# Performance work log

Measured on AMD Instinct MI355X. Metric: run time of the kernel, lower is better.

Reference implementation:

```python
import jax, jax.numpy as jnp
import numpy as np

# dims
B, L, D0, P, K = 4, 512, 640, 128, 16
C, H, NL = 32, 4, 3            # hidden channels, heads, layers
DH = C // H
RAD_IN = P + 2                 # pair feat + bppm + distance
HPT = 0.3                      # high_prob_threshold


def _build_edges(bppm, coords):
    """Backbone + kNN + high-prob edges per sample, deduped, flattened over batch."""
    src_all, dst_all = [], []
    for b in range(B):
        s_bb = np.arange(L - 1); d_bb = np.arange(1, L)
        srcs = [s_bb, d_bb]; dsts = [d_bb, s_bb]
        c = coords[b]
        d2 = ((c[:, None, :] - c[None, :, :]) ** 2).sum(-1)
        nn = np.argsort(d2, axis=1)[:, 1:K + 1]            # exclude self
        s_knn = np.repeat(np.arange(L), K); d_knn = nn.reshape(-1)
        srcs += [s_knn, d_knn]; dsts += [d_knn, s_knn]
        iu, ju = np.triu_indices(L, 2)                      # |i-j| > 1
        m = bppm[b][iu, ju] >= HPT
        hs, hd = iu[m], ju[m]
        srcs += [hs, hd]; dsts += [hd, hs]
        e = np.unique(np.stack([np.concatenate(srcs), np.concatenate(dsts)], 1), axis=0)
        src_all.append(e[:, 0] + b * L); dst_all.append(e[:, 1] + b * L)
    return np.concatenate(src_all).astype(np.int32), np.concatenate(dst_all).astype(np.int32)


def setup_inputs() -> dict:
    rng = np.random.default_rng(0)
    sequence_rep = rng.standard_normal((B, L, D0)).astype(np.float32)
    pair_rep = rng.standard_normal((B, L, L, P)).astype(np.float32)
    u = rng.random((B, L, L)).astype(np.float32)
    bppm = (0.5 * (u + u.transpose(0, 2, 1))) ** 8          # sparse-ish symmetric BPPM
    initial_coords = (10.0 * rng.standard_normal((B, L, 3))).astype(np.float32)
    edge_src, edge_dst = _build_edges(bppm, initial_coords)

    def w(*shape):
        fan = shape[-2] if len(shape) >= 2 else shape[-1]
        return (rng.standard_normal(shape) / np.sqrt(fan)).astype(np.float32)

    inp = dict(
        sequence_rep=jnp.asarray(sequence_rep), pair_rep=jnp.asarray(pair_rep),
        bppm=jnp.asarray(bppm.astype(np.float32)), initial_coords=jnp.asarray(initial_coords),
        edge_src=jnp.asarray(edge_src), edge_dst=jnp.asarray(edge_dst),
        Win0=jnp.asarray(w(D0, C)), Win1=jnp.asarray(w(1, C)),
        Wr1=jnp.asarray(w(NL, RAD_IN, 64)), br1=jnp.zeros((NL, 64), jnp.float32),
        Wr2=jnp.asarray(w(NL, 64, 4 * C)), br2=jnp.zeros((NL, 4 * C), jnp.float32),
        Wm00=jnp.asarray(w(NL, C, C)), Wm01=jnp.asarray(w(NL, C, C)),
        Wm10=jnp.asarray(w(NL, C, C)), Wm11=jnp.asarray(w(NL, C, C)),
        Wq=jnp.asarray(w(NL, C, C)), Wself0=jnp.asarray(w(NL, C, C)), Wself1=jnp.asarray(w(NL, C, C)),
        gamma0=jnp.ones((NL, C), jnp.float32), beta0=jnp.zeros((NL, C), jnp.float32),
        gamma1=jnp.ones((NL, C), jnp.float32), Wout=jnp.asarray(w(C, 1)),
    )
    return inp


def _forward(sequence_rep, pair_rep, bppm, initial_coords,
             Win0, Win1, Wr1, br1, Wr2, br2, Wm00, Wm01, Wm10, Wm11,
             Wq, Wself0, Wself1, gamma0, beta0, gamma1, Wout, edge_src, edge_dst):
    N = B * L
    x = initial_coords.reshape(N, 3)
    h0 = sequence_rep.reshape(N, D0) @ Win0                  # [N,C] degree-0
    h1 = x[:, None, :] * Win1[0][None, :, None]              # [N,C,3] degree-1
    src, dst = edge_src, edge_dst
    rel = x[dst] - x[src]
    r = jnp.sqrt(jnp.sum(rel * rel, -1) + 1e-12)             # [E]
    rhat = rel / (r[:, None] + 1e-8)                         # Y1 spherical harmonic dir
    b_idx, si, di = src // L, src % L, dst % L
    ef = jnp.concatenate([pair_rep[b_idx, si, di], bppm[b_idx, si, di][:, None], r[:, None]], -1)

    for l in range(NL):
        rad = jax.nn.relu(ef @ Wr1[l] + br1[l]) @ Wr2[l] + br2[l]   # [E,4C] radial weights
        w00, w01, w10, w11 = jnp.split(rad, 4, axis=-1)
        h0s, h1s = h0[src], h1[src]
        dot1 = jnp.einsum('ecd,ed->ec', h1s, rhat)                  # deg1 -> deg0 path
        m0 = w00 * (h0s @ Wm00[l]) + w01 * (dot1 @ Wm01[l])          # [E,C]
        m1 = (w11[:, :, None] * jnp.einsum('ecd,cf->efd', h1s, Wm11[l])
              + (w10 * (h0s @ Wm10[l]))[:, :, None] * rhat[:, None, :])  # [E,C,3]
        # multi-head attention over incoming edges
        q = (h0 @ Wq[l]).reshape(N, H, DH)
        k = m0.reshape(-1, H, DH)
        logit = jnp.sum(q[dst] * k, -1) / np.sqrt(DH)                # [E,H]
        mx = jax.ops.segment_max(logit, dst, num_segments=N)
        mx = jnp.where(jnp.isfinite(mx), mx, 0.0)
        a = jnp.exp(logit - mx[dst])
        den = jax.ops.segment_sum(a, dst, num_segments=N)
        alpha = a / (den[dst] + 1e-9)                                # [E,H]
        agg0 = jax.ops.segment_sum(alpha[:, :, None] * k, dst, num_segments=N).reshape(N, C)
        agg1 = jax.ops.segment_sum(alpha[:, :, None, None] * m1.reshape(-1, H, DH, 3),
                                   dst, num_segments=N).reshape(N, C, 3)
        h0 = h0 + agg0 @ Wself0[l]
        h1 = h1 + jnp.einsum('ncd,cf->nfd', agg1, Wself1[l])
        # norms: LayerNorm on deg-0, equivariant norm-gating on deg-1
        mu = h0.mean(-1, keepdims=True)
        h0 = (h0 - mu) / jnp.sqrt(h0.var(-1, keepdims=True) + 1e-5) * gamma0[l] + beta0[l]
        nrm = jnp.sqrt(jnp.sum(h1 * h1, -1) + 1e-12)                 # [N,C]
        nln = (nrm - nrm.mean(-1, keepdims=True)) / jnp.sqrt(nrm.var(-1, keepdims=True) + 1e-5) * gamma1[l]
        h1 = h1 * (nln / (nrm + 1e-8))[:, :, None]
    delta = jnp.einsum('ncd,co->nod', h1, Wout)[:, 0, :]             # fiber_out {'1':1}
    return (x + delta).reshape(B, L, 3)


def reference(sequence_rep, pair_rep, bppm, initial_coords, edge_src, edge_dst,
              Win0, Win1, Wr1, br1, Wr2, br2, Wm00, Wm01, Wm10, Wm11,
              Wq, Wself0, Wself1, gamma0, beta0, gamma1, Wout):
    return _forward(sequence_rep, pair_rep, bppm, initial_coords,
                    Win0, Win1, Wr1, br1, Wr2, br2, Wm00, Wm01, Wm10, Wm11,
                    Wq, Wself0, Wself1, gamma0, beta0, gamma1, Wout, edge_src, edge_dst)
```

## Files before the change

kernel.cpp:

```cpp
#include <hip/hip_runtime.h>
#include <hip/hip_bf16.h>
#include <math.h>

#define BB 4
#define LL 512
#define D0 640
#define PP 128
#define CC 32
#define NLAYER 3
#define NN (BB*LL)
#define RADIN 130

typedef __attribute__((ext_vector_type(8))) short bf16x8;
typedef __attribute__((ext_vector_type(4))) float f32x4;

__device__ __forceinline__ short f2b(float v) {
    __hip_bfloat16 h = __float2bfloat16(v);
    short s; __builtin_memcpy(&s, &h, 2); return s;
}


__global__ __launch_bounds__(64) void k_init_h0(const float* __restrict__ seq,
                                                const float* __restrict__ Win0,
                                                float* __restrict__ h0) {
    const int n = blockIdx.x, lane = threadIdx.x;
    const int c = lane & 31, half = lane >> 5;
    const float* s = seq + (size_t)n * D0;
    float acc = 0.f;
    const int i0 = half * (D0 / 2), i1 = i0 + (D0 / 2);
    for (int i = i0; i < i1; ++i) acc = fmaf(s[i], Win0[i * CC + c], acc);
    acc += __shfl_xor(acc, 32);
    if (lane < 32) h0[n * CC + c] = acc;
}

__global__ void k_init_h1(const float* __restrict__ x, const float* __restrict__ Win1,
                          float* __restrict__ h1, int* __restrict__ deg) {
    int idx = blockIdx.x * blockDim.x + threadIdx.x;
    if (idx < NN) deg[idx] = 0;
    if (idx >= NN * CC) return;
    int n = idx >> 5, c = idx & 31;
    float w = Win1[c];
    const float* xp = x + n * 3;
    float* hp = h1 + (size_t)n * 96 + c * 3;
    hp[0] = xp[0] * w; hp[1] = xp[1] * w; hp[2] = xp[2] * w;
}

__global__ __launch_bounds__(256) void k_edge_setup(
    const int* __restrict__ src, const int* __restrict__ dst,
    const float* __restrict__ x,
    const float* __restrict__ pair, const float* __restrict__ bppm,
    float* __restrict__ rhat, int* __restrict__ deg,
    short* __restrict__ efb, int E)
{
    int e = blockIdx.x * 4 + (threadIdx.x >> 6);
    int lane = threadIdx.x & 63;
    if (e >= E) return;
    int s = src[e], d = dst[e];
    float dx = x[d * 3 + 0] - x[s * 3 + 0];
    float dy = x[d * 3 + 1] - x[s * 3 + 1];
    float dz = x[d * 3 + 2] - x[s * 3 + 2];
    float r = sqrtf(dx * dx + dy * dy + dz * dz + 1e-12f);
    float ir = 1.f / (r + 1e-8f);
    int b = s / LL, si = s % LL, di = d % LL;
    size_t prow = ((size_t)b * LL + si) * LL + di;
    const float* pr = pair + prow * PP;
    short* out = efb + (size_t)e * 160;
    out[lane] = f2b(pr[lane]);
    out[64 + lane] = f2b(pr[64 + lane]);
    if (lane < 32) {
        float v = 0.f;
        if (lane == 0) v = bppm[prow];
        else if (lane == 1) v = r;
        out[128 + lane] = f2b(v);
    }
    if (lane < 3) rhat[e * 3 + lane] = (lane == 0 ? dx : lane == 1 ? dy : dz) * ir;
    if (lane == 0) atomicAdd(&deg[d], 1);
}

__global__ __launch_bounds__(64) void k_scan(const int* __restrict__ deg,
                                             int* __restrict__ rowptr,
                                             int* __restrict__ cursor) {
    const int lane = threadIdx.x;
    const int base = lane * 32;
    int loc[32]; int s = 0;
    for (int i = 0; i < 32; ++i) { loc[i] = deg[base + i]; s += loc[i]; }
    int pre = s;
    for (int off = 1; off < 64; off <<= 1) {
        int t = __shfl_up(pre, off);
        if (lane >= off) pre += t;
    }
    pre -= s;
    int run = pre;
    for (int i = 0; i < 32; ++i) { rowptr[base + i] = run; cursor[base + i] = 0; run += loc[i]; }
    if (lane == 63) rowptr[NN] = run;
}

__global__ void k_scatter(const int* __restrict__ dst, const int* __restrict__ rowptr,
                          int* __restrict__ cursor, int* __restrict__ eperm, int E) {
    int e = blockIdx.x * blockDim.x + threadIdx.x;
    if (e >= E) return;
    int d = dst[e];
    int pos = atomicAdd(&cursor[d], 1);
    eperm[e] = rowptr[d] + pos;
}

__global__ void k_pack(const float* __restrict__ Wr1, const float* __restrict__ Wr2,
                       short* __restrict__ W1p, short* __restrict__ W2p) {
    int t = blockIdx.x * blockDim.x + threadIdx.x;
    const int tot1 = NLAYER * 5 * 4 * 64 * 8;
    const int tot2 = NLAYER * 2 * 8 * 64 * 8;
    if (t < tot1) {
        int j = t & 7; int r = t >> 3;
        int ln = r & 63; r >>= 6;
        int cb = r & 3; r >>= 2;
        int kb = r % 5; int l = r / 5;
        int row = kb * 32 + (ln >> 4) * 8 + j;
        int col = cb * 16 + (ln & 15);
        float v = (row < RADIN) ? Wr1[((size_t)l * RADIN + row) * 64 + col] : 0.f;
        W1p[t] = f2b(v);
    } else if (t < tot1 + tot2) {
        int t2 = t - tot1;
        int j = t2 & 7; int r = t2 >> 3;
        int ln = r & 63; r >>= 6;
        int cb = r & 7; r >>= 3;
        int kb = r & 1; int l = r >> 1;
        int row = kb * 32 + (ln >> 4) * 8 + j;
        int col = cb * 16 + (ln & 15);
        W2p[t2] = f2b(Wr2[((size_t)l * 64 + row) * 128 + col]);
    }
}

__global__ __launch_bounds__(256) void k_nodepre(
    int l, const float* __restrict__ h0, const float* __restrict__ h1,
    const float* __restrict__ Wq, const float* __restrict__ Wm00,
    const float* __restrict__ Wm10, const float* __restrict__ Wm11,
    float* __restrict__ qbuf, float* __restrict__ P00,
    float* __restrict__ P10, float* __restrict__ P11)
{
    __shared__ float sh0[8][32], sh1[8][96];
    const int c = threadIdx.x & 31, hw = threadIdx.x >> 5;
    const int n = blockIdx.x * 8 + hw;
    sh0[hw][c] = h0[n * CC + c];
    const float* hp = h1 + (size_t)n * 96 + c * 3;
    sh1[hw][c * 3 + 0] = hp[0]; sh1[hw][c * 3 + 1] = hp[1]; sh1[hw][c * 3 + 2] = hp[2];
    const float* WqL  = Wq   + l * 1024;
    const float* W00L = Wm00 + l * 1024;
    const float* W10L = Wm10 + l * 1024;
    const float* W11L = Wm11 + l * 1024;
    float q = 0.f, p00 = 0.f, p10 = 0.f, px = 0.f, py = 0.f, pz = 0.f;
    for (int i = 0; i < 32; ++i) {
        float a = sh0[hw][i];
        q   = fmaf(a, WqL[i * 32 + c], q);
        p00 = fmaf(a, W00L[i * 32 + c], p00);
        p10 = fmaf(a, W10L[i * 32 + c], p10);
        float w = W11L[i * 32 + c];
        px = fmaf(sh1[hw][i * 3 + 0], w, px);
        py = fmaf(sh1[hw][i * 3 + 1], w, py);
        pz = fmaf(sh1[hw][i * 3 + 2], w, pz);
    }
    qbuf[n * 32 + c] = q; P00[n * 32 + c] = p00; P10[n * 32 + c] = p10;
    float* pp = P11 + (size_t)n * 96 + c * 3;
    pp[0] = px; pp[1] = py; pp[2] = pz;
}

__global__ __launch_bounds__(256) void k_radedge(
    int l, int E,
    const int* __restrict__ src,
    const float* __restrict__ rhat,
    const short* __restrict__ efb,
    const short* __restrict__ W1p,
    const short* __restrict__ W2p,
    const float* __restrict__ br1,
    const float* __restrict__ br2,
    const float* __restrict__ Wm01,
    const float* __restrict__ h1,
    const float* __restrict__ P00,
    const float* __restrict__ P10,
    const float* __restrict__ P11,
    const int* __restrict__ eperm,
    float* __restrict__ mbuf)
{
    __shared__ short s_hid[4][16][72];
    __shared__ float s_rad[64][132];
    __shared__ float sW[1024];
    const int lane = threadIdx.x & 63, wv = threadIdx.x >> 6;
    const int r16 = lane & 15, q4 = lane >> 4;
    const int eb = blockIdx.x * 64;
    const int e0 = eb + wv * 16;

    for (int i = threadIdx.x; i < 1024; i += 256) sW[i] = Wm01[l * 1024 + i];

    f32x4 acc0 = {0.f,0.f,0.f,0.f}, acc1 = {0.f,0.f,0.f,0.f};
    f32x4 acc2 = {0.f,0.f,0.f,0.f}, acc3 = {0.f,0.f,0.f,0.f};
    int row = e0 + r16; if (row >= E) row = E - 1;
    const short* arow = efb + (size_t)row * 160 + q4 * 8;
    const short* b1b = W1p + (size_t)l * (5 * 4 * 64 * 8) + lane * 8;
    for (int kb = 0; kb < 5; ++kb) {
        bf16x8 af = *(const bf16x8*)(arow + kb * 32);
        const short* bp = b1b + kb * (4 * 64 * 8);
        bf16x8 b0 = *(const bf16x8*)(bp);
        bf16x8 b1v = *(const bf16x8*)(bp + 64 * 8);
        bf16x8 b2v = *(const bf16x8*)(bp + 2 * 64 * 8);
        bf16x8 b3v = *(const bf16x8*)(bp + 3 * 64 * 8);
        acc0 = __builtin_amdgcn_mfma_f32_16x16x32_bf16(af, b0,  acc0, 0, 0, 0);
        acc1 = __builtin_amdgcn_mfma_f32_16x16x32_bf16(af, b1v, acc1, 0, 0, 0);
        acc2 = __builtin_amdgcn_mfma_f32_16x16x32_bf16(af, b2v, acc2, 0, 0, 0);
        acc3 = __builtin_amdgcn_mfma_f32_16x16x32_bf16(af, b3v, acc3, 0, 0, 0);
    }
    {
        f32x4 a[4] = {acc0, acc1, acc2, acc3};
        for (int cb = 0; cb < 4; ++cb) {
            int col = cb * 16 + r16;
            float b = br1[l * 64 + col];
            for (int i = 0; i < 4; ++i) {
                float v = fmaxf(a[cb][i] + b, 0.f);
                s_hid[wv][q4 * 4 + i][col] = f2b(v);
            }
        }
    }
    f32x4 o[8];
    for (int cb = 0; cb < 8; ++cb) { o[cb].x=0.f; o[cb].y=0.f; o[cb].z=0.f; o[cb].w=0.f; }
    const short* b2b = W2p + (size_t)l * (2 * 8 * 64 * 8) + lane * 8;
    for (int kb = 0; kb < 2; ++kb) {
        bf16x8 af = *(const bf16x8*)(&s_hid[wv][r16][kb * 32 + q4 * 8]);
        const short* bp = b2b + kb * (8 * 64 * 8);
        for (int cb = 0; cb < 8; ++cb) {
            bf16x8 bf = *(const bf16x8*)(bp + cb * (64 * 8));
            o[cb] = __builtin_amdgcn_mfma_f32_16x16x32_bf16(af, bf, o[cb], 0, 0, 0);
        }
    }
    for (int cb = 0; cb < 8; ++cb) {
        int col = cb * 16 + r16;
        float b = br2[l * 128 + col];
        for (int i = 0; i < 4; ++i) {
            s_rad[wv * 16 + q4 * 4 + i][col] = o[cb][i] + b;
        }
    }
    __syncthreads();

    const int hw = threadIdx.x >> 5;
    const int c = lane & 31;
    const int base = lane & 32;
    for (int it = 0; it < 8; ++it) {
        const int el = hw * 8 + it;
        const int e = eb + el;
        if (e >= E) break;
        const int s = src[e];
        const float r0 = rhat[e * 3 + 0], r1 = rhat[e * 3 + 1], r2 = rhat[e * 3 + 2];
        const float* hp = h1 + (size_t)s * 96 + c * 3;
        const float dot = hp[0] * r0 + hp[1] * r1 + hp[2] * r2;
        float t1 = 0.f;
        for (int i = 0; i < 32; ++i) {
            float di = __shfl(dot, base + i);
            t1 = fmaf(di, sW[i * 32 + c], t1);
        }
        const float w00 = s_rad[el][c],      w01 = s_rad[el][32 + c];
        const float w10 = s_rad[el][64 + c], w11 = s_rad[el][96 + c];
        const float m0 = fmaf(w00, P00[s * 32 + c], w01 * t1);
        const float u10 = w10 * P10[s * 32 + c];
        const float* pp = P11 + (size_t)s * 96 + c * 3;
        float* mp = mbuf + (size_t)eperm[e] * 128;
        mp[c] = m0;
        mp[32 + c * 3 + 0] = fmaf(w11, pp[0], u10 * r0);
        mp[32 + c * 3 + 1] = fmaf(w11, pp[1], u10 * r1);
        mp[32 + c * 3 + 2] = fmaf(w11, pp[2], u10 * r2);
    }
}

__global__ __launch_bounds__(256) void k_node(
    int l, const int* __restrict__ rowptr,
    const float* __restrict__ mbuf,
    const float* __restrict__ qbuf_in,
    float* __restrict__ h0, float* __restrict__ h1,
    const float* __restrict__ Ws0, const float* __restrict__ Ws1,
    const float* __restrict__ gam0, const float* __restrict__ bet0,
    const float* __restrict__ gam1,
    const float* __restrict__ Wq, const float* __restrict__ Wm00,
    const float* __restrict__ Wm10, const float* __restrict__ Wm11,
    float* __restrict__ qout, float* __restrict__ P00,
    float* __restrict__ P10, float* __restrict__ P11,
    const float* __restrict__ x, const float* __restrict__ Wout,
    float* __restrict__ outp)
{
    const int n = blockIdx.x;
    const int tid = threadIdx.x;
    const int hw = tid >> 5;
    const int c = tid & 31;
    __shared__ float s_part[8][32][6];
    __shared__ float s_a0[32], s_a1[96];
    __shared__ float s_hn[128];

    const float qc = qbuf_in[n * 32 + c];
    const int st = rowptr[n], en = rowptr[n + 1];

    float m_run = -INFINITY, l_run = 0.f;
    float a0 = 0.f, a1x = 0.f, a1y = 0.f, a1z = 0.f;
    for (int idx = st + hw; idx < en; idx += 8) {
        const float* row = mbuf + (size_t)idx * 128;
        const float kc = row[c];
        const float mv0 = row[32 + c * 3 + 0];
        const float mv1 = row[32 + c * 3 + 1];
        const float mv2 = row[32 + c * 3 + 2];
        float p = qc * kc;
        p += __shfl_xor(p, 1); p += __shfl_xor(p, 2); p += __shfl_xor(p, 4);
        const float logit = p * 0.35355339059327373f;
        const float mn = fmaxf(m_run, logit);
        const float sc = __expf(m_run - mn);
        const float w  = __expf(logit - mn);
        l_run = fmaf(l_run, sc, w);
        a0  = fmaf(a0,  sc, w * kc);
        a1x = fmaf(a1x, sc, w * mv0);
        a1y = fmaf(a1y, sc, w * mv1);
        a1z = fmaf(a1z, sc, w * mv2);
        m_run = mn;
    }
    s_part[hw][c][0] = m_run; s_part[hw][c][1] = l_run;
    s_part[hw][c][2] = a0;
    s_part[hw][c][3] = a1x; s_part[hw][c][4] = a1y; s_part[hw][c][5] = a1z;
    __syncthreads();

    if (tid < 32) {
        float M = s_part[0][c][0], L = s_part[0][c][1], A0 = s_part[0][c][2];
        float Ax = s_part[0][c][3], Ay = s_part[0][c][4], Az = s_part[0][c][5];
        for (int k = 1; k < 8; ++k) {
            const float m2 = s_part[k][c][0];
            if (m2 == -INFINITY) continue;
            const float mn = fmaxf(M, m2);
            const float sa = (M == -INFINITY) ? 0.f : __expf(M - mn);
            const float sb = __expf(m2 - mn);
            L  = L  * sa + s_part[k][c][1] * sb;
            A0 = A0 * sa + s_part[k][c][2] * sb;
            Ax = Ax * sa + s_part[k][c][3] * sb;
            Ay = Ay * sa + s_part[k][c][4] * sb;
            Az = Az * sa + s_part[k][c][5] * sb;
            M = mn;
        }
        const float inv = 1.0f / (L + 1e-9f);
        s_a0[c] = A0 * inv;
        s_a1[c * 3 + 0] = Ax * inv;
        s_a1[c * 3 + 1] = Ay * inv;
        s_a1[c * 3 + 2] = Az * inv;
    }
    __syncthreads();

    if (tid < 32) {
        float x0 = h0[n * CC + c];
        {
            const float* W = Ws0 + l * 1024;
            for (int i = 0; i < 32; ++i) x0 = fmaf(s_a0[i], W[i * 32 + c], x0);
        }
        float mu = x0;
        mu += __shfl_xor(mu, 1); mu += __shfl_xor(mu, 2); mu += __shfl_xor(mu, 4);
        mu += __shfl_xor(mu, 8); mu += __shfl_xor(mu, 16);
        mu *= (1.f / 32.f);
        float sq = x0 * x0;
        sq += __shfl_xor(sq, 1); sq += __shfl_xor(sq, 2); sq += __shfl_xor(sq, 4);
        sq += __shfl_xor(sq, 8); sq += __shfl_xor(sq, 16);
        float var = sq * (1.f / 32.f) - mu * mu;
        float h0n = (x0 - mu) * rsqrtf(var + 1e-5f) * gam0[l * 32 + c] + bet0[l * 32 + c];
        s_hn[c] = h0n;
        if (l + 1 < NLAYER) h0[n * CC + c] = h0n;

        const float* hp = h1 + (size_t)n * 96 + c * 3;
        float v0 = hp[0], v1 = hp[1], v2 = hp[2];
        {
            const float* W = Ws1 + l * 1024;
            for (int i = 0; i < 32; ++i) {
                float w = W[i * 32 + c];
                v0 = fmaf(s_a1[i * 3 + 0], w, v0);
                v1 = fmaf(s_a1[i * 3 + 1], w, v1);
                v2 = fmaf(s_a1[i * 3 + 2], w, v2);
            }
        }
        float nrm = sqrtf(v0 * v0 + v1 * v1 + v2 * v2 + 1e-12f);
        float mu2 = nrm;
        mu2 += __shfl_xor(mu2, 1); mu2 += __shfl_xor(mu2, 2); mu2 += __shfl_xor(mu2, 4);
        mu2 += __shfl_xor(mu2, 8); mu2 += __shfl_xor(mu2, 16);
        mu2 *= (1.f / 32.f);
        float sq2 = nrm * nrm;
        sq2 += __shfl_xor(sq2, 1); sq2 += __shfl_xor(sq2, 2); sq2 += __shfl_xor(sq2, 4);
        sq2 += __shfl_xor(sq2, 8); sq2 += __shfl_xor(sq2, 16);
        float var2 = sq2 * (1.f / 32.f) - mu2 * mu2;
        float nln = (nrm - mu2) * rsqrtf(var2 + 1e-5f) * gam1[l * 32 + c];
        float scl = nln / (nrm + 1e-8f);
        float w0 = v0 * scl, w1 = v1 * scl, w2 = v2 * scl;
        s_hn[32 + c * 3 + 0] = w0;
        s_hn[32 + c * 3 + 1] = w1;
        s_hn[32 + c * 3 + 2] = w2;
        if (l + 1 < NLAYER) {
            float* hq = h1 + (size_t)n * 96 + c * 3;
            hq[0] = w0; hq[1] = w1; hq[2] = w2;
        } else {
            const float wo = Wout[c];
            float d0 = w0 * wo, d1 = w1 * wo, d2 = w2 * wo;
            d0 += __shfl_xor(d0, 1); d1 += __shfl_xor(d1, 1); d2 += __shfl_xor(d2, 1);
            d0 += __shfl_xor(d0, 2); d1 += __shfl_xor(d1, 2); d2 += __shfl_xor(d2, 2);
            d0 += __shfl_xor(d0, 4); d1 += __shfl_xor(d1, 4); d2 += __shfl_xor(d2, 4);
            d0 += __shfl_xor(d0, 8); d1 += __shfl_xor(d1, 8); d2 += __shfl_xor(d2, 8);
            d0 += __shfl_xor(d0, 16); d1 += __shfl_xor(d1, 16); d2 += __shfl_xor(d2, 16);
            if (c == 0) {
                outp[n * 3 + 0] = x[n * 3 + 0] + d0;
                outp[n * 3 + 1] = x[n * 3 + 1] + d1;
                outp[n * 3 + 2] = x[n * 3 + 2] + d2;
            }
        }
    }

    if (l + 1 < NLAYER) {
        __syncthreads();
        const int grp = tid >> 5;
        if (grp < 4) {
            const int lp = l + 1;
            if (grp == 0) {
                const float* W = Wq + lp * 1024;
                float acc = 0.f;
                for (int i = 0; i < 32; ++i) acc = fmaf(s_hn[i], W[i * 32 + c], acc);
                qout[n * 32 + c] = acc;
            } else if (grp == 1) {
                const float* W = Wm00 + lp * 1024;
                float acc = 0.f;
                for (int i = 0; i < 32; ++i) acc = fmaf(s_hn[i], W[i * 32 + c], acc);
                P00[n * 32 + c] = acc;
            } else if (grp == 2) {
                const float* W = Wm10 + lp * 1024;
                float acc = 0.f;
                for (int i = 0; i < 32; ++i) acc = fmaf(s_hn[i], W[i * 32 + c], acc);
                P10[n * 32 + c] = acc;
            } else {
                const float* W = Wm11 + lp * 1024;
                float px = 0.f, py = 0.f, pz = 0.f;
                for (int i = 0; i < 32; ++i) {
                    float w = W[i * 32 + c];
                    px = fmaf(s_hn[32 + i * 3 + 0], w, px);
                    py = fmaf(s_hn[32 + i * 3 + 1], w, py);
                    pz = fmaf(s_hn[32 + i * 3 + 2], w, pz);
                }
                float* pp = P11 + (size_t)n * 96 + c * 3;
                pp[0] = px; pp[1] = py; pp[2] = pz;
            }
        }
    }
}

extern "C" void kernel_launch(void* const* d_in, const int* in_sizes, int n_in,
                              void* d_out, int out_size, void* d_ws, size_t ws_size,
                              hipStream_t stream) {
    const float* seq  = (const float*)d_in[0];
    const float* pair = (const float*)d_in[1];
    const float* bppm = (const float*)d_in[2];
    const float* x    = (const float*)d_in[3];
    const int*   src  = (const int*)d_in[4];
    const int*   dst  = (const int*)d_in[5];
    const float* Win0 = (const float*)d_in[6];
    const float* Win1 = (const float*)d_in[7];
    const float* Wr1  = (const float*)d_in[8];
    const float* br1  = (const float*)d_in[9];
    const float* Wr2  = (const float*)d_in[10];
    const float* br2  = (const float*)d_in[11];
    const float* Wm00 = (const float*)d_in[12];
    const float* Wm01 = (const float*)d_in[13];
    const float* Wm10 = (const float*)d_in[14];
    const float* Wm11 = (const float*)d_in[15];
    const float* Wq   = (const float*)d_in[16];
    const float* Ws0  = (const float*)d_in[17];
    const float* Ws1  = (const float*)d_in[18];
    const float* gam0 = (const float*)d_in[19];
    const float* bet0 = (const float*)d_in[20];
    const float* gam1 = (const float*)d_in[21];
    const float* Wout = (const float*)d_in[22];
    const int E = in_sizes[4];

    char* w = (char*)d_ws;
    auto alloc = [&](size_t nbytes) {
        void* p = (void*)w;
        w += (nbytes + 255) & ~(size_t)255;
        return p;
    };
    float* h0    = (float*)alloc((size_t)NN * CC * 4);
    float* h1    = (float*)alloc((size_t)NN * CC * 3 * 4);
    float* rhat  = (float*)alloc((size_t)E * 3 * 4);
    float* mbuf  = (float*)alloc((size_t)E * 128 * 4);
    int* deg     = (int*)alloc((size_t)NN * 4);
    int* rowptr  = (int*)alloc((size_t)(NN + 1) * 4);
    int* cursor  = (int*)alloc((size_t)NN * 4);
    int* eperm   = (int*)alloc((size_t)E * 4);
    short* efb   = (short*)alloc((size_t)E * 160 * 2);
    short* W1p   = (short*)alloc((size_t)NLAYER * 5 * 4 * 64 * 8 * 2);
    short* W2p   = (short*)alloc((size_t)NLAYER * 2 * 8 * 64 * 8 * 2);
    float* qbuf  = (float*)alloc((size_t)NN * 32 * 4);
    float* P00   = (float*)alloc((size_t)NN * 32 * 4);
    float* P10   = (float*)alloc((size_t)NN * 32 * 4);
    float* P11   = (float*)alloc((size_t)NN * 96 * 4);

    const int TB = 256;
    k_init_h0<<<NN, 64, 0, stream>>>(seq, Win0, h0);
    k_init_h1<<<(NN * CC + TB - 1) / TB, TB, 0, stream>>>(x, Win1, h1, deg);
    k_edge_setup<<<(E + 3) / 4, 256, 0, stream>>>(src, dst, x, pair, bppm,
                                                  rhat, deg, efb, E);
    k_scan<<<1, 64, 0, stream>>>(deg, rowptr, cursor);
    k_scatter<<<(E + TB - 1) / TB, TB, 0, stream>>>(dst, rowptr, cursor, eperm, E);
    {
        int tot = NLAYER * 5 * 4 * 64 * 8 + NLAYER * 2 * 8 * 64 * 8;
        k_pack<<<(tot + TB - 1) / TB, TB, 0, stream>>>(Wr1, Wr2, W1p, W2p);
    }
    k_nodepre<<<NN / 8, 256, 0, stream>>>(0, h0, h1, Wq, Wm00, Wm10, Wm11,
                                          qbuf, P00, P10, P11);

    for (int l = 0; l < NLAYER; ++l) {
        k_radedge<<<(E + 63) / 64, 256, 0, stream>>>(l, E, src, rhat, efb, W1p, W2p,
                                                     br1, br2, Wm01, h1,
                                                     P00, P10, P11, eperm, mbuf);
        k_node<<<NN, 256, 0, stream>>>(l, rowptr, mbuf, qbuf, h0, h1,
                                       Ws0, Ws1, gam0, bet0, gam1,
                                       Wq, Wm00, Wm10, Wm11,
                                       qbuf, P00, P10, P11,
                                       x, Wout, (float*)d_out);
    }
}
```

Baseline: 837.1 us.

## Fuse per-edge radial MLP and messages into per-node attention kernel

Merges the per-edge radial-MLP and message kernel into the per-node attention and update kernel. Each node block now gathers its incoming edges through a dst-sorted edge order, computes their radial weights and messages on the fly, and folds them into the online softmax. This drops the E×128 float message buffer and its global write and read traffic, and saves one launch per layer. Node state is double-buffered because other blocks read neighbours' h1 and projections while the node is updated. The trade-off is that MFMA tiles are underfilled for nodes with fewer than 64 edges and work is unbalanced across node blocks.

```diff
diff --git a/kernel.cpp b/kernel.cpp
--- a/kernel.cpp
+++ b/kernel.cpp
@@ -96,12 +96,12 @@
 }
 
 __global__ void k_scatter(const int* __restrict__ dst, const int* __restrict__ rowptr,
-                          int* __restrict__ cursor, int* __restrict__ eperm, int E) {
+                          int* __restrict__ cursor, int* __restrict__ eorder, int E) {
     int e = blockIdx.x * blockDim.x + threadIdx.x;
     if (e >= E) return;
     int d = dst[e];
     int pos = atomicAdd(&cursor[d], 1);
-    eperm[e] = rowptr[d] + pos;
+    eorder[rowptr[d] + pos] = e;
 }
 
 __global__ void k_pack(const float* __restrict__ Wr1, const float* __restrict__ Wr2,
@@ -163,176 +163,168 @@
     pp[0] = px; pp[1] = py; pp[2] = pz;
 }
 
-__global__ __launch_bounds__(256) void k_radedge(
+__global__ __launch_bounds__(256) void k_layer(
     int l, int E,
-    const int* __restrict__ src,
-    const float* __restrict__ rhat,
+    const int* __restrict__ rowptr, const int* __restrict__ eorder,
+    const int* __restrict__ src, const float* __restrict__ rhat,
     const short* __restrict__ efb,
-    const short* __restrict__ W1p,
-    const short* __restrict__ W2p,
-    const float* __restrict__ br1,
-    const float* __restrict__ br2,
+    const short* __restrict__ W1p, const short* __restrict__ W2p,
+    const float* __restrict__ br1, const float* __restrict__ br2,
     const float* __restrict__ Wm01,
-    const float* __restrict__ h1,
-    const float* __restrict__ P00,
-    const float* __restrict__ P10,
-    const float* __restrict__ P11,
-    const int* __restrict__ eperm,
-    float* __restrict__ mbuf)
-{
-    __shared__ short s_hid[4][16][72];
-    __shared__ float s_rad[64][132];
-    __shared__ float sW[1024];
-    const int lane = threadIdx.x & 63, wv = threadIdx.x >> 6;
-    const int r16 = lane & 15, q4 = lane >> 4;
-    const int eb = blockIdx.x * 64;
-    const int e0 = eb + wv * 16;
-
-    for (int i = threadIdx.x; i < 1024; i += 256) sW[i] = Wm01[l * 1024 + i];
-
-    f32x4 acc0 = {0.f,0.f,0.f,0.f}, acc1 = {0.f,0.f,0.f,0.f};
-    f32x4 acc2 = {0.f,0.f,0.f,0.f}, acc3 = {0.f,0.f,0.f,0.f};
-    int row = e0 + r16; if (row >= E) row = E - 1;
-    const short* arow = efb + (size_t)row * 160 + q4 * 8;
-    const short* b1b = W1p + (size_t)l * (5 * 4 * 64 * 8) + lane * 8;
-    for (int kb = 0; kb < 5; ++kb) {
-        bf16x8 af = *(const bf16x8*)(arow + kb * 32);
-        const short* bp = b1b + kb * (4 * 64 * 8);
-        bf16x8 b0 = *(const bf16x8*)(bp);
-        bf16x8 b1v = *(const bf16x8*)(bp + 64 * 8);
-        bf16x8 b2v = *(const bf16x8*)(bp + 2 * 64 * 8);
-        bf16x8 b3v = *(const bf16x8*)(bp + 3 * 64 * 8);
-        acc0 = __builtin_amdgcn_mfma_f32_16x16x32_bf16(af, b0,  acc0, 0, 0, 0);
-        acc1 = __builtin_amdgcn_mfma_f32_16x16x32_bf16(af, b1v, acc1, 0, 0, 0);
-        acc2 = __builtin_amdgcn_mfma_f32_16x16x32_bf16(af, b2v, acc2, 0, 0, 0);
-        acc3 = __builtin_amdgcn_mfma_f32_16x16x32_bf16(af, b3v, acc3, 0, 0, 0);
-    }
-    {
-        f32x4 a[4] = {acc0, acc1, acc2, acc3};
-        for (int cb = 0; cb < 4; ++cb) {
-            int col = cb * 16 + r16;
-            float b = br1[l * 64 + col];
-            for (int i = 0; i < 4; ++i) {
-                float v = fmaxf(a[cb][i] + b, 0.f);
-                s_hid[wv][q4 * 4 + i][col] = f2b(v);
-            }
-        }
-    }
-    f32x4 o[8];
-    for (int cb = 0; cb < 8; ++cb) { o[cb].x=0.f; o[cb].y=0.f; o[cb].z=0.f; o[cb].w=0.f; }
-    const short* b2b = W2p + (size_t)l * (2 * 8 * 64 * 8) + lane * 8;
-    for (int kb = 0; kb < 2; ++kb) {
-        bf16x8 af = *(const bf16x8*)(&s_hid[wv][r16][kb * 32 + q4 * 8]);
-        const short* bp = b2b + kb * (8 * 64 * 8);
-        for (int cb = 0; cb < 8; ++cb) {
-            bf16x8 bf = *(const bf16x8*)(bp + cb * (64 * 8));
-            o[cb] = __builtin_amdgcn_mfma_f32_16x16x32_bf16(af, bf, o[cb], 0, 0, 0);
-        }
-    }
-    for (int cb = 0; cb < 8; ++cb) {
-        int col = cb * 16 + r16;
-        float b = br2[l * 128 + col];
-        for (int i = 0; i < 4; ++i) {
-            s_rad[wv * 16 + q4 * 4 + i][col] = o[cb][i] + b;
-        }
-    }
-    __syncthreads();
-
-    const int hw = threadIdx.x >> 5;
-    const int c = lane & 31;
-    const int base = lane & 32;
-    for (int it = 0; it < 8; ++it) {
-        const int el = hw * 8 + it;
-        const int e = eb + el;
-        if (e >= E) break;
-        const int s = src[e];
-        const float r0 = rhat[e * 3 + 0], r1 = rhat[e * 3 + 1], r2 = rhat[e * 3 + 2];
-        const float* hp = h1 + (size_t)s * 96 + c * 3;
-        const float dot = hp[0] * r0 + hp[1] * r1 + hp[2] * r2;
-        float t1 = 0.f;
-        for (int i = 0; i < 32; ++i) {
-            float di = __shfl(dot, base + i);
-            t1 = fmaf(di, sW[i * 32 + c], t1);
-        }
-        const float w00 = s_rad[el][c],      w01 = s_rad[el][32 + c];
-        const float w10 = s_rad[el][64 + c], w11 = s_rad[el][96 + c];
-        const float m0 = fmaf(w00, P00[s * 32 + c], w01 * t1);
-        const float u10 = w10 * P10[s * 32 + c];
-        const float* pp = P11 + (size_t)s * 96 + c * 3;
-        float* mp = mbuf + (size_t)eperm[e] * 128;
-        mp[c] = m0;
-        mp[32 + c * 3 + 0] = fmaf(w11, pp[0], u10 * r0);
-        mp[32 + c * 3 + 1] = fmaf(w11, pp[1], u10 * r1);
-        mp[32 + c * 3 + 2] = fmaf(w11, pp[2], u10 * r2);
-    }
-}
-
-__global__ __launch_bounds__(256) void k_node(
-    int l, const int* __restrict__ rowptr,
-    const float* __restrict__ mbuf,
-    const float* __restrict__ qbuf_in,
-    float* __restrict__ h0, float* __restrict__ h1,
+    const float* __restrict__ h1_in,
+    const float* __restrict__ P00, const float* __restrict__ P10,
+    const float* __restrict__ P11, const float* __restrict__ qbuf_in,
+    float* __restrict__ h0,
+    float* __restrict__ h1_out,
     const float* __restrict__ Ws0, const float* __restrict__ Ws1,
     const float* __restrict__ gam0, const float* __restrict__ bet0,
     const float* __restrict__ gam1,
     const float* __restrict__ Wq, const float* __restrict__ Wm00,
     const float* __restrict__ Wm10, const float* __restrict__ Wm11,
-    float* __restrict__ qout, float* __restrict__ P00,
-    float* __restrict__ P10, float* __restrict__ P11,
+    float* __restrict__ qout, float* __restrict__ P00o,
+    float* __restrict__ P10o, float* __restrict__ P11o,
     const float* __restrict__ x, const float* __restrict__ Wout,
     float* __restrict__ outp)
 {
     const int n = blockIdx.x;
     const int tid = threadIdx.x;
-    const int hw = tid >> 5;
-    const int c = tid & 31;
-    __shared__ float s_part[8][32][6];
+    const int lane = tid & 63, wv = tid >> 6;
+    const int r16 = lane & 15, q4 = lane >> 4;
+    const int hw = tid >> 5, c = tid & 31;
+
+    __shared__ short s_hid[4][16][72];
+    __shared__ float s_rad[64][132];
+    __shared__ float sW[1024];
+    __shared__ int   s_eid[64];
     __shared__ float s_a0[32], s_a1[96];
     __shared__ float s_hn[128];
-
+#define S_PART(k, cc, j) (((float*)s_rad)[(((k) * 32 + (cc)) * 6) + (j)])
+
+    for (int i = tid; i < 1024; i += 256) sW[i] = Wm01[l * 1024 + i];
+
+    const int st = rowptr[n], en = rowptr[n + 1];
     const float qc = qbuf_in[n * 32 + c];
-    const int st = rowptr[n], en = rowptr[n + 1];
+
+    const short* b1b = W1p + (size_t)l * (5 * 4 * 64 * 8) + lane * 8;
+    const short* b2b = W2p + (size_t)l * (2 * 8 * 64 * 8) + lane * 8;
 
     float m_run = -INFINITY, l_run = 0.f;
     float a0 = 0.f, a1x = 0.f, a1y = 0.f, a1z = 0.f;
-    for (int idx = st + hw; idx < en; idx += 8) {
-        const float* row = mbuf + (size_t)idx * 128;
-        const float kc = row[c];
-        const float mv0 = row[32 + c * 3 + 0];
-        const float mv1 = row[32 + c * 3 + 1];
-        const float mv2 = row[32 + c * 3 + 2];
-        float p = qc * kc;
-        p += __shfl_xor(p, 1); p += __shfl_xor(p, 2); p += __shfl_xor(p, 4);
-        const float logit = p * 0.35355339059327373f;
-        const float mn = fmaxf(m_run, logit);
-        const float sc = __expf(m_run - mn);
-        const float w  = __expf(logit - mn);
-        l_run = fmaf(l_run, sc, w);
-        a0  = fmaf(a0,  sc, w * kc);
-        a1x = fmaf(a1x, sc, w * mv0);
-        a1y = fmaf(a1y, sc, w * mv1);
-        a1z = fmaf(a1z, sc, w * mv2);
-        m_run = mn;
-    }
-    s_part[hw][c][0] = m_run; s_part[hw][c][1] = l_run;
-    s_part[hw][c][2] = a0;
-    s_part[hw][c][3] = a1x; s_part[hw][c][4] = a1y; s_part[hw][c][5] = a1z;
+
+    for (int t0 = st; t0 < en; t0 += 64) {
+        __syncthreads();
+        if (tid < 64) {
+            int slot = t0 + tid;
+            s_eid[tid] = eorder[slot < en ? slot : en - 1];
+        }
+        __syncthreads();
+
+        f32x4 acc0 = {0.f,0.f,0.f,0.f}, acc1 = {0.f,0.f,0.f,0.f};
+        f32x4 acc2 = {0.f,0.f,0.f,0.f}, acc3 = {0.f,0.f,0.f,0.f};
+        {
+            const int eid = s_eid[wv * 16 + r16];
+            const short* arow = efb + (size_t)eid * 160 + q4 * 8;
+            for (int kb = 0; kb < 5; ++kb) {
+                bf16x8 af = *(const bf16x8*)(arow + kb * 32);
+                const short* bp = b1b + kb * (4 * 64 * 8);
+                bf16x8 b0 = *(const bf16x8*)(bp);
+                bf16x8 b1v = *(const bf16x8*)(bp + 64 * 8);
+                bf16x8 b2v = *(const bf16x8*)(bp + 2 * 64 * 8);
+                bf16x8 b3v = *(const bf16x8*)(bp + 3 * 64 * 8);
+                acc0 = __builtin_amdgcn_mfma_f32_16x16x32_bf16(af, b0,  acc0, 0, 0, 0);
+                acc1 = __builtin_amdgcn_mfma_f32_16x16x32_bf16(af, b1v, acc1, 0, 0, 0);
+                acc2 = __builtin_amdgcn_mfma_f32_16x16x32_bf16(af, b2v, acc2, 0, 0, 0);
+                acc3 = __builtin_amdgcn_mfma_f32_16x16x32_bf16(af, b3v, acc3, 0, 0, 0);
+            }
+        }
+        {
+            f32x4 a[4] = {acc0, acc1, acc2, acc3};
+            for (int cb = 0; cb < 4; ++cb) {
+                int col = cb * 16 + r16;
+                float b = br1[l * 64 + col];
+                for (int i = 0; i < 4; ++i) {
+                    float v = fmaxf(a[cb][i] + b, 0.f);
+                    s_hid[wv][q4 * 4 + i][col] = f2b(v);
+                }
+            }
+        }
+        f32x4 o[8];
+        for (int cb = 0; cb < 8; ++cb) { o[cb].x=0.f; o[cb].y=0.f; o[cb].z=0.f; o[cb].w=0.f; }
+        for (int kb = 0; kb < 2; ++kb) {
+            bf16x8 af = *(const bf16x8*)(&s_hid[wv][r16][kb * 32 + q4 * 8]);
+            const short* bp = b2b + kb * (8 * 64 * 8);
+            for (int cb = 0; cb < 8; ++cb) {
+                bf16x8 bf = *(const bf16x8*)(bp + cb * (64 * 8));
+                o[cb] = __builtin_amdgcn_mfma_f32_16x16x32_bf16(af, bf, o[cb], 0, 0, 0);
+            }
+        }
+        for (int cb = 0; cb < 8; ++cb) {
+            int col = cb * 16 + r16;
+            float b = br2[l * 128 + col];
+            for (int i = 0; i < 4; ++i) {
+                s_rad[wv * 16 + q4 * 4 + i][col] = o[cb][i] + b;
+            }
+        }
+        __syncthreads();
+
+        const int base = lane & 32;
+        for (int it = 0; it < 8; ++it) {
+            const int el = hw * 8 + it;
+            const int slot = t0 + el;
+            if (slot >= en) break;
+            const int e = s_eid[el];
+            const int s = src[e];
+            const float r0 = rhat[e * 3 + 0], r1 = rhat[e * 3 + 1], r2 = rhat[e * 3 + 2];
+            const float* hp = h1_in + (size_t)s * 96 + c * 3;
+            const float dot = hp[0] * r0 + hp[1] * r1 + hp[2] * r2;
+            float t1 = 0.f;
+            for (int i = 0; i < 32; ++i) {
+                float di = __shfl(dot, base + i);
+                t1 = fmaf(di, sW[i * 32 + c], t1);
+            }
+            const float w00 = s_rad[el][c],      w01 = s_rad[el][32 + c];
+            const float w10 = s_rad[el][64 + c], w11 = s_rad[el][96 + c];
+            const float kc = fmaf(w00, P00[s * 32 + c], w01 * t1);
+            const float u10 = w10 * P10[s * 32 + c];
+            const float* pp = P11 + (size_t)s * 96 + c * 3;
+            const float mv0 = fmaf(w11, pp[0], u10 * r0);
+            const float mv1 = fmaf(w11, pp[1], u10 * r1);
+            const float mv2 = fmaf(w11, pp[2], u10 * r2);
+            float p = qc * kc;
+            p += __shfl_xor(p, 1); p += __shfl_xor(p, 2); p += __shfl_xor(p, 4);
+            const float logit = p * 0.35355339059327373f;
+            const float mn = fmaxf(m_run, logit);
+            const float sc = __expf(m_run - mn);
+            const float w  = __expf(logit - mn);
+            l_run = fmaf(l_run, sc, w);
+            a0  = fmaf(a0,  sc, w * kc);
+            a1x = fmaf(a1x, sc, w * mv0);
+            a1y = fmaf(a1y, sc, w * mv1);
+            a1z = fmaf(a1z, sc, w * mv2);
+            m_run = mn;
+        }
+    }
+
     __syncthreads();
+    S_PART(hw, c, 0) = m_run; S_PART(hw, c, 1) = l_run;
+    S_PART(hw, c, 2) = a0;
+    S_PART(hw, c, 3) = a1x; S_PART(hw, c, 4) = a1y; S_PART(hw, c, 5) = a1z;
+    __syncthreads();
 
     if (tid < 32) {
-        float M = s_part[0][c][0], L = s_part[0][c][1], A0 = s_part[0][c][2];
-        float Ax = s_part[0][c][3], Ay = s_part[0][c][4], Az = s_part[0][c][5];
+        float M = S_PART(0, c, 0), L = S_PART(0, c, 1), A0 = S_PART(0, c, 2);
+        float Ax = S_PART(0, c, 3), Ay = S_PART(0, c, 4), Az = S_PART(0, c, 5);
         for (int k = 1; k < 8; ++k) {
-            const float m2 = s_part[k][c][0];
+            const float m2 = S_PART(k, c, 0);
             if (m2 == -INFINITY) continue;
             const float mn = fmaxf(M, m2);
             const float sa = (M == -INFINITY) ? 0.f : __expf(M - mn);
             const float sb = __expf(m2 - mn);
-            L  = L  * sa + s_part[k][c][1] * sb;
-            A0 = A0 * sa + s_part[k][c][2] * sb;
-            Ax = Ax * sa + s_part[k][c][3] * sb;
-            Ay = Ay * sa + s_part[k][c][4] * sb;
-            Az = Az * sa + s_part[k][c][5] * sb;
+            L  = L  * sa + S_PART(k, c, 1) * sb;
+            A0 = A0 * sa + S_PART(k, c, 2) * sb;
+            Ax = Ax * sa + S_PART(k, c, 3) * sb;
+            Ay = Ay * sa + S_PART(k, c, 4) * sb;
+            Az = Az * sa + S_PART(k, c, 5) * sb;
             M = mn;
         }
         const float inv = 1.0f / (L + 1e-9f);
@@ -361,7 +353,7 @@
         s_hn[c] = h0n;
         if (l + 1 < NLAYER) h0[n * CC + c] = h0n;
 
-        const float* hp = h1 + (size_t)n * 96 + c * 3;
+        const float* hp = h1_in + (size_t)n * 96 + c * 3;
         float v0 = hp[0], v1 = hp[1], v2 = hp[2];
         {
             const float* W = Ws1 + l * 1024;
@@ -388,7 +380,7 @@
         s_hn[32 + c * 3 + 1] = w1;
         s_hn[32 + c * 3 + 2] = w2;
         if (l + 1 < NLAYER) {
-            float* hq = h1 + (size_t)n * 96 + c * 3;
+            float* hq = h1_out + (size_t)n * 96 + c * 3;
             hq[0] = w0; hq[1] = w1; hq[2] = w2;
         } else {
             const float wo = Wout[c];
@@ -420,12 +412,12 @@
                 const float* W = Wm00 + lp * 1024;
                 float acc = 0.f;
                 for (int i = 0; i < 32; ++i) acc = fmaf(s_hn[i], W[i * 32 + c], acc);
-                P00[n * 32 + c] = acc;
+                P00o[n * 32 + c] = acc;
             } else if (grp == 2) {
                 const float* W = Wm10 + lp * 1024;
                 float acc = 0.f;
                 for (int i = 0; i < 32; ++i) acc = fmaf(s_hn[i], W[i * 32 + c], acc);
-                P10[n * 32 + c] = acc;
+                P10o[n * 32 + c] = acc;
             } else {
                 const float* W = Wm11 + lp * 1024;
                 float px = 0.f, py = 0.f, pz = 0.f;
@@ -435,11 +427,12 @@
                     py = fmaf(s_hn[32 + i * 3 + 1], w, py);
                     pz = fmaf(s_hn[32 + i * 3 + 2], w, pz);
                 }
-                float* pp = P11 + (size_t)n * 96 + c * 3;
+                float* pp = P11o + (size_t)n * 96 + c * 3;
                 pp[0] = px; pp[1] = py; pp[2] = pz;
             }
         }
     }
+#undef S_PART
 }
 
 extern "C" void kernel_launch(void* const* d_in, const int* in_sizes, int n_in,
@@ -477,43 +470,54 @@
         return p;
     };
     float* h0    = (float*)alloc((size_t)NN * CC * 4);
-    float* h1    = (float*)alloc((size_t)NN * CC * 3 * 4);
+    float* h1a   = (float*)alloc((size_t)NN * 96 * 4);
+    float* h1b   = (float*)alloc((size_t)NN * 96 * 4);
     float* rhat  = (float*)alloc((size_t)E * 3 * 4);
-    float* mbuf  = (float*)alloc((size_t)E * 128 * 4);
     int* deg     = (int*)alloc((size_t)NN * 4);
     int* rowptr  = (int*)alloc((size_t)(NN + 1) * 4);
     int* cursor  = (int*)alloc((size_t)NN * 4);
-    int* eperm   = (int*)alloc((size_t)E * 4);
+    int* eorder  = (int*)alloc((size_t)E * 4);
     short* efb   = (short*)alloc((size_t)E * 160 * 2);
     short* W1p   = (short*)alloc((size_t)NLAYER * 5 * 4 * 64 * 8 * 2);
     short* W2p   = (short*)alloc((size_t)NLAYER * 2 * 8 * 64 * 8 * 2);
-    float* qbuf  = (float*)alloc((size_t)NN * 32 * 4);
-    float* P00   = (float*)alloc((size_t)NN * 32 * 4);
-    float* P10   = (float*)alloc((size_t)NN * 32 * 4);
-    float* P11   = (float*)alloc((size_t)NN * 96 * 4);
+    float* qbufA = (float*)alloc((size_t)NN * 32 * 4);
+    float* qbufB = (float*)alloc((size_t)NN * 32 * 4);
+    float* P00A  = (float*)alloc((size_t)NN * 32 * 4);
+    float* P00B  = (float*)alloc((size_t)NN * 32 * 4);
+    float* P10A  = (float*)alloc((size_t)NN * 32 * 4);
+    float* P10B  = (float*)alloc((size_t)NN * 32 * 4);
+    float* P11A  = (float*)alloc((size_t)NN * 96 * 4);
+    float* P11B  = (float*)alloc((size_t)NN * 96 * 4);
+
+    float* h1_[2]  = {h1a, h1b};
+    float* q_[2]   = {qbufA, qbufB};
+    float* p00_[2] = {P00A, P00B};
+    float* p10_[2] = {P10A, P10B};
+    float* p11_[2] = {P11A, P11B};
 
     const int TB = 256;
     k_init_h0<<<NN, 64, 0, stream>>>(seq, Win0, h0);
-    k_init_h1<<<(NN * CC + TB - 1) / TB, TB, 0, stream>>>(x, Win1, h1, deg);
+    k_init_h1<<<(NN * CC + TB - 1) / TB, TB, 0, stream>>>(x, Win1, h1a, deg);
     k_edge_setup<<<(E + 3) / 4, 256, 0, stream>>>(src, dst, x, pair, bppm,
                                                   rhat, deg, efb, E);
     k_scan<<<1, 64, 0, stream>>>(deg, rowptr, cursor);
-    k_scatter<<<(E + TB - 1) / TB, TB, 0, stream>>>(dst, rowptr, cursor, eperm, E);
+    k_scatter<<<(E + TB - 1) / TB, TB, 0, stream>>>(dst, rowptr, cursor, eorder, E);
     {
         int tot = NLAYER * 5 * 4 * 64 * 8 + NLAYER * 2 * 8 * 64 * 8;
         k_pack<<<(tot + TB - 1) / TB, TB, 0, stream>>>(Wr1, Wr2, W1p, W2p);
     }
-    k_nodepre<<<NN / 8, 256, 0, stream>>>(0, h0, h1, Wq, Wm00, Wm10, Wm11,
-                                          qbuf, P00, P10, P11);
+    k_nodepre<<<NN / 8, 256, 0, stream>>>(0, h0, h1a, Wq, Wm00, Wm10, Wm11,
+                                          qbufA, P00A, P10A, P11A);
 
     for (int l = 0; l < NLAYER; ++l) {
-        k_radedge<<<(E + 63) / 64, 256, 0, stream>>>(l, E, src, rhat, efb, W1p, W2p,
-                                                     br1, br2, Wm01, h1,
-                                                     P00, P10, P11, eperm, mbuf);
-        k_node<<<NN, 256, 0, stream>>>(l, rowptr, mbuf, qbuf, h0, h1,
-                                       Ws0, Ws1, gam0, bet0, gam1,
-                                       Wq, Wm00, Wm10, Wm11,
-                                       qbuf, P00, P10, P11,
-                                       x, Wout, (float*)d_out);
-    }
-}
+        const int in = l & 1, out = (l + 1) & 1;
+        k_layer<<<NN, 256, 0, stream>>>(
+            l, E, rowptr, eorder, src, rhat, efb, W1p, W2p, br1, br2,
+            Wm01, h1_[in], p00_[in], p10_[in], p11_[in], q_[in],
+            h0, h1_[out],
+            Ws0, Ws1, gam0, bet0, gam1,
+            Wq, Wm00, Wm10, Wm11,
+            q_[out], p00_[out], p10_[out], p11_[out],
+            x, Wout, (float*)d_out);
+    }
+}
```

New measurement: 1.225 ms. +46.3%, slower.
